# Performance work log

Measured on AMD Instinct MI355X. Metric: run time of the kernel, lower is better.

The kernel has to match this reference:

```python
import jax, jax.numpy as jnp
import numpy as np

N = 50000   # nodes
E = 800000  # edges
D = 64      # hidden_layer_size
L = 4       # depth
EPS = 1e-5


def setup_inputs() -> dict:
    key = jax.random.key(0)
    ks = jax.random.split(key, 24)
    def g(k, shape, scale=0.05):
        return (jax.random.normal(k, shape, dtype=jnp.float32) * scale)
    inp = {
        "x": jax.random.normal(ks[0], (N, 2), dtype=jnp.float32),
        "edge_attr": jax.random.normal(ks[1], (E, 1), dtype=jnp.float32),
        "edge_index": jax.random.randint(ks[2], (2, E), 0, N),
        # input projections
        "hp_w": g(ks[3], (2, D)), "hp_b": jnp.zeros((D,), jnp.float32),
        "ep_w": g(ks[4], (1, D)), "ep_b": jnp.zeros((D,), jnp.float32),
        # per-layer GatedGCN-style linears, stacked over depth L
        "Uw": g(ks[5], (L, D, D)), "Ub": jnp.zeros((L, D), jnp.float32),
        "Vw": g(ks[6], (L, D, D)), "Vb": jnp.zeros((L, D), jnp.float32),
        "Aw": g(ks[7], (L, D, D)), "Ab": jnp.zeros((L, D), jnp.float32),
        "Bw": g(ks[8], (L, D, D)), "Bb": jnp.zeros((L, D), jnp.float32),
        "Cw": g(ks[9], (L, D, D)), "Cb": jnp.zeros((L, D), jnp.float32),
        # batchnorm affine params per layer
        "hg": jnp.ones((L, D), jnp.float32), "hb": jnp.zeros((L, D), jnp.float32),
        "eg": jnp.ones((L, D), jnp.float32), "eb": jnp.zeros((L, D), jnp.float32),
        # feature extractor MLP [D, D, D, 1]
        "f1w": g(ks[10], (D, D)), "f1b": jnp.zeros((D,), jnp.float32),
        "f2w": g(ks[11], (D, D)), "f2b": jnp.zeros((D,), jnp.float32),
        "f3w": g(ks[12], (D, 1)), "f3b": jnp.zeros((1,), jnp.float32),
    }
    return inp


def _batchnorm(v, gamma, beta):
    # training-mode BN over the batch (row) dimension
    m = v.mean(axis=0)
    var = v.var(axis=0)
    return (v - m) * jax.lax.rsqrt(var + EPS) * gamma + beta


def _segment_mean(vals, seg, num_segments):
    sums = jax.ops.segment_sum(vals, seg, num_segments=num_segments)
    cnt = jax.ops.segment_sum(jnp.ones((vals.shape[0],), vals.dtype), seg,
                              num_segments=num_segments)
    return sums / jnp.maximum(cnt, 1.0)[:, None]


def reference(x, edge_attr, edge_index, hp_w, hp_b, ep_w, ep_b,
              Uw, Ub, Vw, Vb, Aw, Ab, Bw, Bb, Cw, Cb,
              hg, hb, eg, eb, f1w, f1b, f2w, f2b, f3w, f3b):
    n = x.shape[0]
    dst = edge_index[0]  # aggregation target / Bh gather index
    src = edge_index[1]  # Vh / Ch gather index

    h = jax.nn.relu(x @ hp_w + hp_b)          # [N, D]
    e = jax.nn.relu(edge_attr @ ep_w + ep_b)  # [E, D]

    for l in range(L):
        h_in, e_in = h, e
        Uh = h @ Uw[l] + Ub[l]
        Vh = h @ Vw[l] + Vb[l]
        Ae = e @ Aw[l] + Ab[l]
        Bh = h @ Bw[l] + Bb[l]
        Ch = h @ Cw[l] + Cb[l]
        gate = jax.nn.sigmoid(e_in)                      # [E, D]
        agg = _segment_mean(gate * Vh[src], dst, n)      # [N, D]
        h = h_in + jax.nn.relu(_batchnorm(Uh + agg, hg[l], hb[l]))
        e = e_in + jax.nn.relu(_batchnorm(Ae + Bh[dst] + Ch[src], eg[l], eb[l]))

    # feature extractor MLP: silu, silu, sigmoid
    z = jax.nn.silu(e @ f1w + f1b)
    z = jax.nn.silu(z @ f2w + f2b)
    out = jax.nn.sigmoid(z @ f3w + f3b)  # [E, 1]
    return out
```

## Files before the change

kernel.cpp:

```cpp
#include <hip/hip_runtime.h>

#define NNODE 50000
#define NEDGE 800000
#define NLAYER 4
#define BN_EPS 1e-5f

#define NH (NNODE*64)
#define NE (NEDGE*64)
#define NBUCKET 256

typedef __attribute__((ext_vector_type(8))) short short8v;
typedef unsigned short us;

__device__ __forceinline__ float sigf(float x){ return 1.0f/(1.0f+__expf(-x)); }

__device__ __forceinline__ float bf2f(us u){
  union { unsigned int i; float f; } c; c.i = ((unsigned int)u)<<16; return c.f;
}
__device__ __forceinline__ us f2bf(float f){
  union { float f; unsigned int i; } c; c.f = f;
  unsigned int r = c.i + 0x7FFFu + ((c.i>>16)&1u);
  return (us)(r>>16);
}
__device__ __forceinline__ float hf2f(us u){
  union { us u; _Float16 h; } c; c.u=u; return (float)c.h;
}
__device__ __forceinline__ us f2hf(float f){
  union { us u; _Float16 h; } c; c.h=(_Float16)f; return c.u;
}

__global__ void k_zero_i(int* __restrict__ p, int n){
  int i = blockIdx.x*256 + threadIdx.x;
  if(i<n) p[i]=0;
}
__global__ void k_zero_f(float* __restrict__ p, int n){
  int i = blockIdx.x*256 + threadIdx.x;
  if(i<n) p[i]=0.f;
}
__global__ void k_count(const int* __restrict__ ei, int* __restrict__ cnt){
  int i = blockIdx.x*256 + threadIdx.x;
  if(i<NEDGE) atomicAdd(&cnt[ei[i]], 1);
}
__global__ void k_inv(const int* __restrict__ cnt, float* __restrict__ invc){
  int i = blockIdx.x*256 + threadIdx.x;
  if(i<NNODE){ int c=cnt[i]; invc[i] = 1.0f/(float)(c<1?1:c); }
}

__global__ void k_scan(const int* __restrict__ cnt, int* __restrict__ row_ptr,
                       int* __restrict__ cursor){
  __shared__ int buf[256];
  __shared__ int carry;
  const int tid = threadIdx.x;
  if(tid==0) carry=0;
  __syncthreads();
  for(int base=0; base<NNODE; base+=256){
    int i = base+tid;
    int v = (i<NNODE)? cnt[i] : 0;
    buf[tid]=v; __syncthreads();
    #pragma unroll
    for(int off=1; off<256; off<<=1){
      int t = (tid>=off)? buf[tid-off] : 0;
      __syncthreads();
      buf[tid]+=t;
      __syncthreads();
    }
    int excl = carry + buf[tid]-v;
    if(i<NNODE){ row_ptr[i]=excl; cursor[i]=excl; }
    __syncthreads();
    if(tid==0) carry += buf[255];
    __syncthreads();
  }
  if(tid==0) row_ptr[NNODE]=carry;
}

__global__ void k_fill(const int* __restrict__ ei, int* __restrict__ cursor,
                       int* __restrict__ eidP){
  int i = blockIdx.x*256 + threadIdx.x;
  if(i<NEDGE){
    int pos = atomicAdd(&cursor[ei[i]], 1);
    eidP[pos] = i;
  }
}

__global__ void k_perm(const int* __restrict__ ei, const int* __restrict__ eidP,
                       int* __restrict__ dstP, int* __restrict__ srcP){
  int p = blockIdx.x*256 + threadIdx.x;
  if(p<NEDGE){
    int eid = eidP[p];
    dstP[p] = ei[eid];
    srcP[p] = ei[NEDGE+eid];
  }
}

__global__ void k_init_h(const float* __restrict__ x, const float* __restrict__ w,
                         const float* __restrict__ b, float* __restrict__ h){
  int t = blockIdx.x*256 + threadIdx.x;
  if(t>=NH) return;
  int i=t>>6, j=t&63;
  float v = x[2*i]*w[j] + x[2*i+1]*w[64+j] + b[j];
  h[t] = fmaxf(v, 0.0f);
}

__global__ void k_init_e(const float* __restrict__ ea, const int* __restrict__ eidP,
                         const float* __restrict__ w, const float* __restrict__ b,
                         us* __restrict__ e){
  int t = blockIdx.x*256 + threadIdx.x;
  if(t >= NE/2) return;
  int p = t>>5;
  int j = (t&31)<<1;
  float a = ea[eidP[p]];
  float v0 = fmaxf(a*w[j]   + b[j],   0.f);
  float v1 = fmaxf(a*w[j+1] + b[j+1], 0.f);
  unsigned int pk = (unsigned int)f2bf(v0) | ((unsigned int)f2bf(v1)<<16);
  *reinterpret_cast<unsigned int*>(&e[2*t]) = pk;
}

__device__ __forceinline__ void tile_gemm(const float (&At)[64][68], const float (&Ws)[64][68],
                                          int r0, int c0, float (&acc)[4][4]){
  #pragma unroll 4
  for(int k=0;k<64;++k){
    const float4 a = *reinterpret_cast<const float4*>(&At[k][r0]);
    const float4 b = *reinterpret_cast<const float4*>(&Ws[k][c0]);
    const float av[4]={a.x,a.y,a.z,a.w};
    const float bv[4]={b.x,b.y,b.z,b.w};
    #pragma unroll
    for(int ri=0;ri<4;++ri)
      #pragma unroll
      for(int ci=0;ci<4;++ci)
        acc[ri][ci] = fmaf(av[ri], bv[ci], acc[ri][ci]);
  }
}

__device__ __forceinline__ void tile_gemm_hW(const float (&At)[64][68], const us (&Wh)[64][68],
                                             int r0, int c0, float (&acc)[4][4]){
  #pragma unroll 4
  for(int k=0;k<64;++k){
    const float4 a = *reinterpret_cast<const float4*>(&At[k][r0]);
    const ushort4 b = *reinterpret_cast<const ushort4*>(&Wh[k][c0]);
    const float av[4]={a.x,a.y,a.z,a.w};
    const float bv[4]={hf2f(b.x),hf2f(b.y),hf2f(b.z),hf2f(b.w)};
    #pragma unroll
    for(int ri=0;ri<4;++ri)
      #pragma unroll
      for(int ci=0;ci<4;++ci)
        acc[ri][ci] = fmaf(av[ri], bv[ci], acc[ri][ci]);
  }
}

__device__ __forceinline__ void stage_At_f32(float (&At)[64][68], const float* __restrict__ src,
                                             int row0, int rowmax, int tid){
  for(int it=0; it<4; ++it){
    int idx = tid + it*256;
    int r = idx>>4, c4=(idx&15)<<2;
    int gr = row0 + r;
    float4 v = make_float4(0.f,0.f,0.f,0.f);
    if(gr < rowmax) v = *reinterpret_cast<const float4*>(&src[(size_t)gr*64 + c4]);
    At[c4+0][r]=v.x; At[c4+1][r]=v.y; At[c4+2][r]=v.z; At[c4+3][r]=v.w;
  }
}

__device__ __forceinline__ void stage_At_bf16(float (&At)[64][68], const us* __restrict__ src,
                                              int row0, int tid){
  #pragma unroll
  for(int it=0; it<2; ++it){
    int idx = tid + it*256;
    int r = idx>>3, c8 = (idx&7)<<3;
    int gr = row0 + r;
    const short8v v = *reinterpret_cast<const short8v*>(&src[(size_t)gr*64 + c8]);
    #pragma unroll
    for(int j=0;j<8;++j) At[c8+j][r] = bf2f((us)v[j]);
  }
}

__device__ __forceinline__ void stage_W(float (&Ws)[64][68], const float* __restrict__ W, int tid){
  for(int it=0; it<4; ++it){
    int idx = tid + it*256;
    int k = idx>>4, c4=(idx&15)<<2;
    *reinterpret_cast<float4*>(&Ws[k][c4]) = *reinterpret_cast<const float4*>(&W[k*64+c4]);
  }
}

__device__ __forceinline__ void stage_Wh(us (&Wh)[64][68], const float* __restrict__ W, int tid){
  for(int it=0; it<4; ++it){
    int idx = tid + it*256;
    int k = idx>>4, c4=(idx&15)<<2;
    const float4 w = *reinterpret_cast<const float4*>(&W[k*64+c4]);
    ushort4 o;
    o.x=f2hf(w.x); o.y=f2hf(w.y); o.z=f2hf(w.z); o.w=f2hf(w.w);
    *reinterpret_cast<ushort4*>(&Wh[k][c4]) = o;
  }
}

__device__ __forceinline__ void node_one_mat_f32(float (&At)[64][68], float (&Ws)[64][68],
    const float* __restrict__ W, const float* __restrict__ B, float* __restrict__ O,
    int row0, int tid){
  __syncthreads();
  stage_W(Ws, W, tid);
  __syncthreads();
  const int tx=tid&15, ty=tid>>4, r0=tx<<2, c0=ty<<2;
  float acc[4][4]={{0.f}};
  tile_gemm(At, Ws, r0, c0, acc);
  const float4 b4 = *reinterpret_cast<const float4*>(&B[c0]);
  const float bb[4]={b4.x,b4.y,b4.z,b4.w};
  #pragma unroll
  for(int ri=0;ri<4;++ri){
    int gr = row0 + r0 + ri;
    if(gr < NNODE){
      float4 o = make_float4(acc[ri][0]+bb[0], acc[ri][1]+bb[1],
                             acc[ri][2]+bb[2], acc[ri][3]+bb[3]);
      *reinterpret_cast<float4*>(&O[(size_t)gr*64 + c0]) = o;
    }
  }
}

__device__ __forceinline__ void node_one_mat_f16(float (&At)[64][68], float (&Ws)[64][68],
    const float* __restrict__ W, const float* __restrict__ B, us* __restrict__ O,
    int row0, int tid){
  __syncthreads();
  stage_W(Ws, W, tid);
  __syncthreads();
  const int tx=tid&15, ty=tid>>4, r0=tx<<2, c0=ty<<2;
  float acc[4][4]={{0.f}};
  tile_gemm(At, Ws, r0, c0, acc);
  const float4 b4 = *reinterpret_cast<const float4*>(&B[c0]);
  const float bb[4]={b4.x,b4.y,b4.z,b4.w};
  #pragma unroll
  for(int ri=0;ri<4;++ri){
    int gr = row0 + r0 + ri;
    if(gr < NNODE){
      unsigned int p0 = (unsigned int)f2hf(acc[ri][0]+bb[0]) | ((unsigned int)f2hf(acc[ri][1]+bb[1])<<16);
      unsigned int p1 = (unsigned int)f2hf(acc[ri][2]+bb[2]) | ((unsigned int)f2hf(acc[ri][3]+bb[3])<<16);
      *reinterpret_cast<uint2*>(&O[(size_t)gr*64 + c0]) = make_uint2(p0,p1);
    }
  }
}

__global__ __launch_bounds__(256) void k_node_gemm(
    const float* __restrict__ h,
    const float* __restrict__ Uw, const float* __restrict__ Ub,
    const float* __restrict__ Vw, const float* __restrict__ Vb,
    const float* __restrict__ Bw, const float* __restrict__ Bb,
    const float* __restrict__ Cw, const float* __restrict__ Cb,
    float* __restrict__ Uh, us* __restrict__ Vh,
    us* __restrict__ Bh, us* __restrict__ Ch)
{
  __shared__ float At[64][68];
  __shared__ float Ws[64][68];
  const int tid = threadIdx.x;
  const int row0 = blockIdx.x*64;
  stage_At_f32(At, h, row0, NNODE, tid);
  node_one_mat_f32(At, Ws, Uw, Ub, Uh, row0, tid);
  node_one_mat_f16(At, Ws, Vw, Vb, Vh, row0, tid);
  node_one_mat_f16(At, Ws, Bw, Bb, Bh, row0, tid);
  node_one_mat_f16(At, Ws, Cw, Cb, Ch, row0, tid);
}

__global__ __launch_bounds__(256) void k_edge_A(
    const us* __restrict__ e,
    const float* __restrict__ Aw, const float* __restrict__ Ab,
    const us* __restrict__ Bh, const us* __restrict__ Ch,
    const int* __restrict__ dstP, const int* __restrict__ srcP,
    us* __restrict__ t16, float* __restrict__ buckets)
{
  __shared__ float At[64][68];
  __shared__ us    Wh[64][68];
  __shared__ float red[128];
  const int tid=threadIdx.x;
  const int row0 = blockIdx.x*64;
  if(tid<128) red[tid]=0.f;
  const int tx=tid&15, ty=tid>>4, r0=tx<<2, c0=ty<<2;
  int dstI[4], srcI[4];
  #pragma unroll
  for(int ri=0;ri<4;++ri){
    dstI[ri]=dstP[row0+r0+ri];
    srcI[ri]=srcP[row0+r0+ri];
  }
  stage_At_bf16(At, e, row0, tid);
  stage_Wh(Wh, Aw, tid);
  __syncthreads();
  uint2 bh2[4], ch2[4];
  #pragma unroll
  for(int ri=0;ri<4;++ri){
    bh2[ri] = *reinterpret_cast<const uint2*>(&Bh[(size_t)dstI[ri]*64 + c0]);
    ch2[ri] = *reinterpret_cast<const uint2*>(&Ch[(size_t)srcI[ri]*64 + c0]);
  }
  float acc[4][4]={{0.f}};
  tile_gemm_hW(At, Wh, r0, c0, acc);

  const float4 ab4 = *reinterpret_cast<const float4*>(&Ab[c0]);
  const float ab[4]={ab4.x,ab4.y,ab4.z,ab4.w};

  float s1[4]={0.f,0.f,0.f,0.f}, s2[4]={0.f,0.f,0.f,0.f};
  #pragma unroll
  for(int ri=0;ri<4;++ri){
    const float bh[4]={hf2f((us)(bh2[ri].x&0xffff)), hf2f((us)(bh2[ri].x>>16)),
                       hf2f((us)(bh2[ri].y&0xffff)), hf2f((us)(bh2[ri].y>>16))};
    const float ch[4]={hf2f((us)(ch2[ri].x&0xffff)), hf2f((us)(ch2[ri].x>>16)),
                       hf2f((us)(ch2[ri].y&0xffff)), hf2f((us)(ch2[ri].y>>16))};
    float tv[4];
    #pragma unroll
    for(int ci=0;ci<4;++ci){
      float t = acc[ri][ci] + ab[ci] + bh[ci] + ch[ci];
      tv[ci]=t;
      s1[ci]+=t; s2[ci]+=t*t;
    }
    unsigned int p0 = (unsigned int)f2hf(tv[0]) | ((unsigned int)f2hf(tv[1])<<16);
    unsigned int p1 = (unsigned int)f2hf(tv[2]) | ((unsigned int)f2hf(tv[3])<<16);
    *reinterpret_cast<uint2*>(&t16[(size_t)(row0+r0+ri)*64 + c0]) = make_uint2(p0,p1);
  }
  #pragma unroll
  for(int ci=0;ci<4;++ci){
    atomicAdd(&red[c0+ci],    s1[ci]);
    atomicAdd(&red[64+c0+ci], s2[ci]);
  }
  __syncthreads();
  float* bk = buckets + (size_t)(blockIdx.x & (NBUCKET-1))*256;
  if(tid<128) atomicAdd(&bk[tid], red[tid]);
}

__global__ __launch_bounds__(256) void k_agg(
    const us* __restrict__ e,
    const us* __restrict__ Vh,
    const int* __restrict__ srcP,
    const int* __restrict__ row_ptr,
    const float* __restrict__ invc,
    float* __restrict__ Uh, float* __restrict__ buckets)
{
  __shared__ float red[128];
  const int tid=threadIdx.x;
  if(tid<128) red[tid]=0.f;
  __syncthreads();
  const int lane = tid&63;
  const int node = blockIdx.x*4 + (tid>>6);
  const int beg = row_ptr[node];
  const int end = row_ptr[node+1];
  float acc = 0.f;
  int p = beg;
  for(; p+4<=end; p+=4){
    int s0=srcP[p], s1i=srcP[p+1], s2i=srcP[p+2], s3=srcP[p+3];
    float v0=hf2f(Vh[(size_t)s0*64 + lane]);
    float v1=hf2f(Vh[(size_t)s1i*64 + lane]);
    float v2=hf2f(Vh[(size_t)s2i*64 + lane]);
    float v3=hf2f(Vh[(size_t)s3*64 + lane]);
    float e0=bf2f(e[(size_t)(p+0)*64 + lane]);
    float e1=bf2f(e[(size_t)(p+1)*64 + lane]);
    float e2=bf2f(e[(size_t)(p+2)*64 + lane]);
    float e3=bf2f(e[(size_t)(p+3)*64 + lane]);
    acc = fmaf(sigf(e0), v0, acc);
    acc = fmaf(sigf(e1), v1, acc);
    acc = fmaf(sigf(e2), v2, acc);
    acc = fmaf(sigf(e3), v3, acc);
  }
  for(; p<end; ++p){
    int src = srcP[p];
    float g = sigf(bf2f(e[(size_t)p*64 + lane]));
    acc = fmaf(g, hf2f(Vh[(size_t)src*64 + lane]), acc);
  }
  size_t o = (size_t)node*64 + lane;
  float val = Uh[o] + acc*invc[node];
  Uh[o] = val;
  atomicAdd(&red[lane], val);
  atomicAdd(&red[64+lane], val*val);
  __syncthreads();
  float* bk = buckets + (size_t)(blockIdx.x & (NBUCKET-1))*256;
  if(tid<128) atomicAdd(&bk[128+tid], red[tid]);
}

__global__ void k_redstats(const float* __restrict__ buckets, float* __restrict__ stats){
  const int tid = threadIdx.x;
  float s = 0.f;
  for(int b=0;b<NBUCKET;++b) s += buckets[(size_t)b*256 + tid];
  stats[tid] = s;
}

__global__ void k_node_finB(const float* __restrict__ th, float* __restrict__ h,
                            const float* __restrict__ stats,
                            const float* __restrict__ hg, const float* __restrict__ hb){
  int t = blockIdx.x*256 + threadIdx.x;
  if(t>=NH) return;
  int j=t&63;
  const float invN = 1.0f/(float)NNODE;
  float mean = stats[128+j]*invN;
  float var  = stats[192+j]*invN - mean*mean;
  float rstd = rsqrtf(var + BN_EPS);
  float v = (th[t]-mean)*rstd*hg[j] + hb[j];
  h[t] += fmaxf(v, 0.0f);
}

__global__ __launch_bounds__(256) void k_ebn(
    const us* __restrict__ t16,
    const float* __restrict__ stats,
    const float* __restrict__ eg, const float* __restrict__ eb,
    us* __restrict__ e)
{
  __shared__ float a_s[64], b_s[64];
  const int tid=threadIdx.x;
  if(tid<64){
    const float invE = 1.0f/(float)NEDGE;
    float mean = stats[tid]*invE;
    float var  = stats[64+tid]*invE - mean*mean;
    float rstd = rsqrtf(var + BN_EPS);
    float a = rstd*eg[tid];
    a_s[tid]=a;
    b_s[tid]=eb[tid]-mean*a;
  }
  __syncthreads();
  size_t idx = (size_t)blockIdx.x*256 + tid;
  int j0 = ((int)idx&7)<<3;
  const short8v tv = *reinterpret_cast<const short8v*>(&t16[idx*8]);
  const short8v ev = *reinterpret_cast<const short8v*>(&e[idx*8]);
  short8v ov;
  #pragma unroll
  for(int j=0;j<8;++j){
    float tt = hf2f((us)tv[j]);
    float v  = tt*a_s[j0+j] + b_s[j0+j];
    float o  = bf2f((us)ev[j]) + fmaxf(v, 0.0f);
    ov[j] = (short)f2bf(o);
  }
  *reinterpret_cast<short8v*>(&e[idx*8]) = ov;
}

__global__ __launch_bounds__(256) void k_mlp(
    const us* __restrict__ e,
    const int* __restrict__ eidP,
    const float* __restrict__ f1w, const float* __restrict__ f1b,
    const float* __restrict__ f2w, const float* __restrict__ f2b,
    const float* __restrict__ f3w, const float* __restrict__ f3b,
    float* __restrict__ out)
{
  __shared__ float At[64][68];
  __shared__ float Ws[64][68];
  __shared__ float ored[64];
  const int tid=threadIdx.x;
  const int row0 = blockIdx.x*64;
  if(tid<64) ored[tid]=0.f;
  stage_At_bf16(At, e, row0, tid);
  stage_W(Ws, f1w, tid);
  __syncthreads();
  const int tx=tid&15, ty=tid>>4, r0=tx<<2, c0=ty<<2;
  float acc[4][4]={{0.f}};
  tile_gemm(At, Ws, r0, c0, acc);
  const float4 b14 = *reinterpret_cast<const float4*>(&f1b[c0]);
  const float b1[4]={b14.x,b14.y,b14.z,b14.w};
  float z1[4][4];
  #pragma unroll
  for(int ri=0;ri<4;++ri)
    #pragma unroll
    for(int ci=0;ci<4;++ci){
      float v = acc[ri][ci]+b1[ci];
      z1[ri][ci] = v*sigf(v);
    }
  __syncthreads();
  #pragma unroll
  for(int ri=0;ri<4;++ri)
    #pragma unroll
    for(int ci=0;ci<4;++ci)
      At[c0+ci][r0+ri] = z1[ri][ci];
  stage_W(Ws, f2w, tid);
  __syncthreads();
  float acc2[4][4]={{0.f}};
  tile_gemm(At, Ws, r0, c0, acc2);
  const float4 b24 = *reinterpret_cast<const float4*>(&f2b[c0]);
  const float b2[4]={b24.x,b24.y,b24.z,b24.w};
  const float4 w34 = *reinterpret_cast<const float4*>(&f3w[c0]);
  const float w3[4]={w34.x,w34.y,w34.z,w34.w};
  float part[4]={0.f,0.f,0.f,0.f};
  #pragma unroll
  for(int ri=0;ri<4;++ri)
    #pragma unroll
    for(int ci=0;ci<4;++ci){
      float v = acc2[ri][ci]+b2[ci];
      float z = v*sigf(v);
      part[ri] += z*w3[ci];
    }
  #pragma unroll
  for(int ri=0;ri<4;++ri) atomicAdd(&ored[r0+ri], part[ri]);
  __syncthreads();
  if(tid<64) out[eidP[row0+tid]] = sigf(ored[tid] + f3b[0]);
}

extern "C" void kernel_launch(void* const* d_in, const int* in_sizes, int n_in,
                              void* d_out, int out_size, void* d_ws, size_t ws_size,
                              hipStream_t stream){
  const float* x    = (const float*)d_in[0];
  const float* ea   = (const float*)d_in[1];
  const int*   ei   = (const int*)  d_in[2];
  const float* hp_w = (const float*)d_in[3];
  const float* hp_b = (const float*)d_in[4];
  const float* ep_w = (const float*)d_in[5];
  const float* ep_b = (const float*)d_in[6];
  const float* Uw   = (const float*)d_in[7];
  const float* Ub   = (const float*)d_in[8];
  const float* Vw   = (const float*)d_in[9];
  const float* Vb   = (const float*)d_in[10];
  const float* Aw   = (const float*)d_in[11];
  const float* Ab   = (const float*)d_in[12];
  const float* Bw   = (const float*)d_in[13];
  const float* Bb   = (const float*)d_in[14];
  const float* Cw   = (const float*)d_in[15];
  const float* Cb   = (const float*)d_in[16];
  const float* hg   = (const float*)d_in[17];
  const float* hb   = (const float*)d_in[18];
  const float* eg   = (const float*)d_in[19];
  const float* eb   = (const float*)d_in[20];
  const float* f1w  = (const float*)d_in[21];
  const float* f1b  = (const float*)d_in[22];
  const float* f2w  = (const float*)d_in[23];
  const float* f2b  = (const float*)d_in[24];
  const float* f3w  = (const float*)d_in[25];
  const float* f3b  = (const float*)d_in[26];

  char* base = (char*)d_ws;
  us* e    = (us*)base;
  us* t16  = (us*)(base + (size_t)NE*2);
  float* h  = (float*)(base + 2ull*NE*2);
  float* Uh = h + (size_t)NH;
  float* stats = Uh + (size_t)NH;
  float* buckets = stats + 256;
  us* Vh = (us*)(buckets + NBUCKET*256);
  us* Bh = Vh + (size_t)NH;
  us* Ch = Bh + (size_t)NH;
  int* cnt     = (int*)(Ch + (size_t)NH);
  float* invc  = (float*)(cnt + NNODE);
  int* row_ptr = (int*)(invc + NNODE);
  int* cursor  = row_ptr + NNODE + 1;
  int* eidP    = cursor + NNODE;
  int* dstP    = eidP + NEDGE;
  int* srcP    = dstP + NEDGE;

  dim3 blk(256);
  k_zero_i<<<dim3((NNODE+255)/256), blk, 0, stream>>>(cnt, NNODE);
  k_count <<<dim3((NEDGE+255)/256), blk, 0, stream>>>(ei, cnt);
  k_inv   <<<dim3((NNODE+255)/256), blk, 0, stream>>>(cnt, invc);
  k_scan  <<<dim3(1), blk, 0, stream>>>(cnt, row_ptr, cursor);
  k_fill  <<<dim3((NEDGE+255)/256), blk, 0, stream>>>(ei, cursor, eidP);
  k_perm  <<<dim3((NEDGE+255)/256), blk, 0, stream>>>(ei, eidP, dstP, srcP);
  k_init_h<<<dim3((NH+255)/256), blk, 0, stream>>>(x, hp_w, hp_b, h);
  k_init_e<<<dim3((NE/2+255)/256), blk, 0, stream>>>(ea, eidP, ep_w, ep_b, e);

  for(int l=0;l<NLAYER;++l){
    k_zero_f<<<dim3(NBUCKET*256/256), blk, 0, stream>>>(buckets, NBUCKET*256);
    k_node_gemm<<<dim3((NNODE+63)/64), blk, 0, stream>>>(h,
        Uw+l*4096, Ub+l*64, Vw+l*4096, Vb+l*64,
        Bw+l*4096, Bb+l*64, Cw+l*4096, Cb+l*64,
        Uh, Vh, Bh, Ch);
    k_edge_A<<<dim3(NEDGE/64), blk, 0, stream>>>(e, Aw+l*4096, Ab+l*64,
        Bh, Ch, dstP, srcP, t16, buckets);
    k_agg<<<dim3(NNODE/4), blk, 0, stream>>>(e, Vh, srcP, row_ptr,
        invc, Uh, buckets);
    k_redstats<<<dim3(1), blk, 0, stream>>>(buckets, stats);
    k_node_finB<<<dim3(NH/256), blk, 0, stream>>>(Uh, h, stats, hg+l*64, hb+l*64);
    k_ebn<<<dim3(NE/8/256), blk, 0, stream>>>(t16, stats, eg+l*64, eb+l*64, e);
  }
  k_mlp<<<dim3(NEDGE/64), blk, 0, stream>>>(e, eidP, f1w, f1b, f2w, f2b,
                                            f3w, f3b, (float*)d_out);
}
```

Before: 2.345 ms.

## Split node GEMM across blocks per matrix and widen edge GEMM tiles

```diff
diff --git a/kernel.cpp b/kernel.cpp
--- a/kernel.cpp
+++ b/kernel.cpp
@@ -8,6 +8,7 @@
 #define NH (NNODE*64)
 #define NE (NEDGE*64)
 #define NBUCKET 256
+#define NGB 782
 
 typedef __attribute__((ext_vector_type(8))) short short8v;
 typedef unsigned short us;
@@ -131,22 +132,6 @@
   }
 }
 
-__device__ __forceinline__ void tile_gemm_hW(const float (&At)[64][68], const us (&Wh)[64][68],
-                                             int r0, int c0, float (&acc)[4][4]){
-  #pragma unroll 4
-  for(int k=0;k<64;++k){
-    const float4 a = *reinterpret_cast<const float4*>(&At[k][r0]);
-    const ushort4 b = *reinterpret_cast<const ushort4*>(&Wh[k][c0]);
-    const float av[4]={a.x,a.y,a.z,a.w};
-    const float bv[4]={hf2f(b.x),hf2f(b.y),hf2f(b.z),hf2f(b.w)};
-    #pragma unroll
-    for(int ri=0;ri<4;++ri)
-      #pragma unroll
-      for(int ci=0;ci<4;++ci)
-        acc[ri][ci] = fmaf(av[ri], bv[ci], acc[ri][ci]);
-  }
-}
-
 __device__ __forceinline__ void stage_At_f32(float (&At)[64][68], const float* __restrict__ src,
                                              int row0, int rowmax, int tid){
   for(int it=0; it<4; ++it){
@@ -188,50 +173,6 @@
     ushort4 o;
     o.x=f2hf(w.x); o.y=f2hf(w.y); o.z=f2hf(w.z); o.w=f2hf(w.w);
     *reinterpret_cast<ushort4*>(&Wh[k][c4]) = o;
-  }
-}
-
-__device__ __forceinline__ void node_one_mat_f32(float (&At)[64][68], float (&Ws)[64][68],
-    const float* __restrict__ W, const float* __restrict__ B, float* __restrict__ O,
-    int row0, int tid){
-  __syncthreads();
-  stage_W(Ws, W, tid);
-  __syncthreads();
-  const int tx=tid&15, ty=tid>>4, r0=tx<<2, c0=ty<<2;
-  float acc[4][4]={{0.f}};
-  tile_gemm(At, Ws, r0, c0, acc);
-  const float4 b4 = *reinterpret_cast<const float4*>(&B[c0]);
-  const float bb[4]={b4.x,b4.y,b4.z,b4.w};
-  #pragma unroll
-  for(int ri=0;ri<4;++ri){
-    int gr = row0 + r0 + ri;
-    if(gr < NNODE){
-      float4 o = make_float4(acc[ri][0]+bb[0], acc[ri][1]+bb[1],
-                             acc[ri][2]+bb[2], acc[ri][3]+bb[3]);
-      *reinterpret_cast<float4*>(&O[(size_t)gr*64 + c0]) = o;
-    }
-  }
-}
-
-__device__ __forceinline__ void node_one_mat_f16(float (&At)[64][68], float (&Ws)[64][68],
-    const float* __restrict__ W, const float* __restrict__ B, us* __restrict__ O,
-    int row0, int tid){
-  __syncthreads();
-  stage_W(Ws, W, tid);
-  __syncthreads();
-  const int tx=tid&15, ty=tid>>4, r0=tx<<2, c0=ty<<2;
-  float acc[4][4]={{0.f}};
-  tile_gemm(At, Ws, r0, c0, acc);
-  const float4 b4 = *reinterpret_cast<const float4*>(&B[c0]);
-  const float bb[4]={b4.x,b4.y,b4.z,b4.w};
-  #pragma unroll
-  for(int ri=0;ri<4;++ri){
-    int gr = row0 + r0 + ri;
-    if(gr < NNODE){
-      unsigned int p0 = (unsigned int)f2hf(acc[ri][0]+bb[0]) | ((unsigned int)f2hf(acc[ri][1]+bb[1])<<16);
-      unsigned int p1 = (unsigned int)f2hf(acc[ri][2]+bb[2]) | ((unsigned int)f2hf(acc[ri][3]+bb[3])<<16);
-      *reinterpret_cast<uint2*>(&O[(size_t)gr*64 + c0]) = make_uint2(p0,p1);
-    }
   }
 }
 
@@ -247,12 +188,41 @@
   __shared__ float At[64][68];
   __shared__ float Ws[64][68];
   const int tid = threadIdx.x;
-  const int row0 = blockIdx.x*64;
+  const int bid = blockIdx.x;
+  const int mat = bid / NGB;
+  const int row0 = (bid % NGB)*64;
+  const float* W = (mat==0)? Uw : (mat==1)? Vw : (mat==2)? Bw : Cw;
+  const float* B = (mat==0)? Ub : (mat==1)? Vb : (mat==2)? Bb : Cb;
   stage_At_f32(At, h, row0, NNODE, tid);
-  node_one_mat_f32(At, Ws, Uw, Ub, Uh, row0, tid);
-  node_one_mat_f16(At, Ws, Vw, Vb, Vh, row0, tid);
-  node_one_mat_f16(At, Ws, Bw, Bb, Bh, row0, tid);
-  node_one_mat_f16(At, Ws, Cw, Cb, Ch, row0, tid);
+  stage_W(Ws, W, tid);
+  __syncthreads();
+  const int tx=tid&15, ty=tid>>4, r0=tx<<2, c0=ty<<2;
+  float acc[4][4]={{0.f}};
+  tile_gemm(At, Ws, r0, c0, acc);
+  const float4 b4 = *reinterpret_cast<const float4*>(&B[c0]);
+  const float bb[4]={b4.x,b4.y,b4.z,b4.w};
+  if(mat==0){
+    #pragma unroll
+    for(int ri=0;ri<4;++ri){
+      int gr = row0 + r0 + ri;
+      if(gr < NNODE){
+        float4 o = make_float4(acc[ri][0]+bb[0], acc[ri][1]+bb[1],
+                               acc[ri][2]+bb[2], acc[ri][3]+bb[3]);
+        *reinterpret_cast<float4*>(&Uh[(size_t)gr*64 + c0]) = o;
+      }
+    }
+  } else {
+    us* O = (mat==1)? Vh : (mat==2)? Bh : Ch;
+    #pragma unroll
+    for(int ri=0;ri<4;++ri){
+      int gr = row0 + r0 + ri;
+      if(gr < NNODE){
+        unsigned int p0 = (unsigned int)f2hf(acc[ri][0]+bb[0]) | ((unsigned int)f2hf(acc[ri][1]+bb[1])<<16);
+        unsigned int p1 = (unsigned int)f2hf(acc[ri][2]+bb[2]) | ((unsigned int)f2hf(acc[ri][3]+bb[3])<<16);
+        *reinterpret_cast<uint2*>(&O[(size_t)gr*64 + c0]) = make_uint2(p0,p1);
+      }
+    }
+  }
 }
 
 __global__ __launch_bounds__(256) void k_edge_A(
@@ -262,41 +232,54 @@
     const int* __restrict__ dstP, const int* __restrict__ srcP,
     us* __restrict__ t16, float* __restrict__ buckets)
 {
-  __shared__ float At[64][68];
+  __shared__ us    Ats[64][136];
   __shared__ us    Wh[64][68];
   __shared__ float red[128];
   const int tid=threadIdx.x;
-  const int row0 = blockIdx.x*64;
+  const int row0 = blockIdx.x*128;
   if(tid<128) red[tid]=0.f;
-  const int tx=tid&15, ty=tid>>4, r0=tx<<2, c0=ty<<2;
-  int dstI[4], srcI[4];
-  #pragma unroll
-  for(int ri=0;ri<4;++ri){
-    dstI[ri]=dstP[row0+r0+ri];
-    srcI[ri]=srcP[row0+r0+ri];
-  }
-  stage_At_bf16(At, e, row0, tid);
+  #pragma unroll
+  for(int it=0; it<4; ++it){
+    int idx = tid + it*256;
+    int r = idx>>3, c8 = (idx&7)<<3;
+    const short8v v = *reinterpret_cast<const short8v*>(&e[(size_t)(row0+r)*64 + c8]);
+    #pragma unroll
+    for(int j=0;j<8;++j) Ats[c8+j][r] = (us)v[j];
+  }
   stage_Wh(Wh, Aw, tid);
   __syncthreads();
-  uint2 bh2[4], ch2[4];
-  #pragma unroll
-  for(int ri=0;ri<4;++ri){
-    bh2[ri] = *reinterpret_cast<const uint2*>(&Bh[(size_t)dstI[ri]*64 + c0]);
-    ch2[ri] = *reinterpret_cast<const uint2*>(&Ch[(size_t)srcI[ri]*64 + c0]);
-  }
-  float acc[4][4]={{0.f}};
-  tile_gemm_hW(At, Wh, r0, c0, acc);
+
+  const int tx=tid&15, ty=tid>>4, r0=tx<<3, c0=ty<<2;
+  float acc[8][4]={{0.f}};
+  #pragma unroll 2
+  for(int k=0;k<64;++k){
+    const short8v a = *reinterpret_cast<const short8v*>(&Ats[k][r0]);
+    const ushort4 b = *reinterpret_cast<const ushort4*>(&Wh[k][c0]);
+    const float bv[4]={hf2f(b.x),hf2f(b.y),hf2f(b.z),hf2f(b.w)};
+    #pragma unroll
+    for(int ri=0;ri<8;++ri){
+      const float av = bf2f((us)a[ri]);
+      #pragma unroll
+      for(int ci=0;ci<4;++ci)
+        acc[ri][ci] = fmaf(av, bv[ci], acc[ri][ci]);
+    }
+  }
 
   const float4 ab4 = *reinterpret_cast<const float4*>(&Ab[c0]);
   const float ab[4]={ab4.x,ab4.y,ab4.z,ab4.w};
 
   float s1[4]={0.f,0.f,0.f,0.f}, s2[4]={0.f,0.f,0.f,0.f};
   #pragma unroll
-  for(int ri=0;ri<4;++ri){
-    const float bh[4]={hf2f((us)(bh2[ri].x&0xffff)), hf2f((us)(bh2[ri].x>>16)),
-                       hf2f((us)(bh2[ri].y&0xffff)), hf2f((us)(bh2[ri].y>>16))};
-    const float ch[4]={hf2f((us)(ch2[ri].x&0xffff)), hf2f((us)(ch2[ri].x>>16)),
-                       hf2f((us)(ch2[ri].y&0xffff)), hf2f((us)(ch2[ri].y>>16))};
+  for(int ri=0;ri<8;++ri){
+    const int slot = row0 + r0 + ri;
+    const int dstI = dstP[slot];
+    const int srcI = srcP[slot];
+    const uint2 b2 = *reinterpret_cast<const uint2*>(&Bh[(size_t)dstI*64 + c0]);
+    const uint2 c2 = *reinterpret_cast<const uint2*>(&Ch[(size_t)srcI*64 + c0]);
+    const float bh[4]={hf2f((us)(b2.x&0xffff)), hf2f((us)(b2.x>>16)),
+                       hf2f((us)(b2.y&0xffff)), hf2f((us)(b2.y>>16))};
+    const float ch[4]={hf2f((us)(c2.x&0xffff)), hf2f((us)(c2.x>>16)),
+                       hf2f((us)(c2.y&0xffff)), hf2f((us)(c2.y>>16))};
     float tv[4];
     #pragma unroll
     for(int ci=0;ci<4;++ci){
@@ -306,7 +289,7 @@
     }
     unsigned int p0 = (unsigned int)f2hf(tv[0]) | ((unsigned int)f2hf(tv[1])<<16);
     unsigned int p1 = (unsigned int)f2hf(tv[2]) | ((unsigned int)f2hf(tv[3])<<16);
-    *reinterpret_cast<uint2*>(&t16[(size_t)(row0+r0+ri)*64 + c0]) = make_uint2(p0,p1);
+    *reinterpret_cast<uint2*>(&t16[(size_t)slot*64 + c0]) = make_uint2(p0,p1);
   }
   #pragma unroll
   for(int ci=0;ci<4;++ci){
@@ -366,10 +349,13 @@
   if(tid<128) atomicAdd(&bk[128+tid], red[tid]);
 }
 
-__global__ void k_redstats(const float* __restrict__ buckets, float* __restrict__ stats){
+__global__ void k_redstats(float* __restrict__ buckets, float* __restrict__ stats){
   const int tid = threadIdx.x;
   float s = 0.f;
-  for(int b=0;b<NBUCKET;++b) s += buckets[(size_t)b*256 + tid];
+  for(int b=0;b<NBUCKET;++b){
+    s += buckets[(size_t)b*256 + tid];
+    buckets[(size_t)b*256 + tid] = 0.f;
+  }
   stats[tid] = s;
 }
 
@@ -537,14 +523,14 @@
   k_perm  <<<dim3((NEDGE+255)/256), blk, 0, stream>>>(ei, eidP, dstP, srcP);
   k_init_h<<<dim3((NH+255)/256), blk, 0, stream>>>(x, hp_w, hp_b, h);
   k_init_e<<<dim3((NE/2+255)/256), blk, 0, stream>>>(ea, eidP, ep_w, ep_b, e);
+  k_zero_f<<<dim3(NBUCKET*256/256), blk, 0, stream>>>(buckets, NBUCKET*256);
 
   for(int l=0;l<NLAYER;++l){
-    k_zero_f<<<dim3(NBUCKET*256/256), blk, 0, stream>>>(buckets, NBUCKET*256);
-    k_node_gemm<<<dim3((NNODE+63)/64), blk, 0, stream>>>(h,
+    k_node_gemm<<<dim3(NGB*4), blk, 0, stream>>>(h,
         Uw+l*4096, Ub+l*64, Vw+l*4096, Vb+l*64,
         Bw+l*4096, Bb+l*64, Cw+l*4096, Cb+l*64,
         Uh, Vh, Bh, Ch);
-    k_edge_A<<<dim3(NEDGE/64), blk, 0, stream>>>(e, Aw+l*4096, Ab+l*64,
+    k_edge_A<<<dim3(NEDGE/128), blk, 0, stream>>>(e, Aw+l*4096, Ab+l*64,
         Bh, Ch, dstP, srcP, t16, buckets);
     k_agg<<<dim3(NNODE/4), blk, 0, stream>>>(e, Vh, srcP, row_ptr,
         invc, Uh, buckets);
```

Result: faster. 2.016 ms (-14.0%).
